# Optimization experiments

Hardware: AMD Instinct MI355X
Metric: run time of the kernel (lower is better)

## Reference

```python
import jax, jax.numpy as jnp
import numpy as np

DIM = 1024
N_HEADS = 16
HEAD_DIM = DIM // N_HEADS  # 64
HALF = HEAD_DIM // 2       # 32
DEPTH = 6
N_BRANCH = 2
NEG_INF = -1e9


def _rot_H(x, cos, sin, m):
    # H direction: adjacent-pair complex layout (..., HALF, 2)
    # x: [B,S,H,D], cos/sin: [HALF], m: [B,S] int
    B, S, H, D = x.shape
    xr = x.reshape(B, S, H, HALF, 2)
    re, im = xr[..., 0], xr[..., 1]
    re2 = re * cos - im * sin
    im2 = re * sin + im * cos
    rot = jnp.stack([re2, im2], axis=-1).reshape(B, S, H, D)
    return jnp.where((m != 0)[:, :, None, None], rot, x)


def _rot_B(x, cos, sin, m):
    # B direction: split-half complex layout (real = first half, imag = second half)
    re, im = x[..., :HALF], x[..., HALF:]
    re2 = re * cos - im * sin
    im2 = re * sin + im * cos
    rot = jnp.concatenate([re2, im2], axis=-1)
    return jnp.where((m != 0)[:, :, None, None], rot, x)


def _apply_rope_instructions(x, H_mask, B_mask, freqs_cos, freqs_sin):
    # Sequentially compose rotations per depth level, as in the torch loops.
    for i in range(DEPTH):
        x = _rot_H(x, freqs_cos[1], freqs_sin[1], H_mask[i])
        for b in range(N_BRANCH):
            x = _rot_B(x, freqs_cos[b + 1], freqs_sin[b + 1], B_mask[i, b])
    return x


def setup_inputs() -> dict:
    key = jax.random.key(0)
    ks = jax.random.split(key, 10)
    B, S = 2, 1024
    x = jax.random.normal(ks[0], (B, S, DIM), dtype=jnp.float32)
    masks = jax.random.randint(ks[1], (B, 1, S, S), 0, 2, dtype=jnp.int32)
    H_mask = jax.random.randint(ks[2], (DEPTH, B, S), 0, 2, dtype=jnp.int32)
    B_mask = jax.random.randint(ks[3], (DEPTH, N_BRANCH, B, S), 0, 2, dtype=jnp.int32)
    theta = jax.random.uniform(ks[4], (4, HALF), dtype=jnp.float32) * 2.0 * np.pi
    freqs_cos = jnp.cos(theta)
    freqs_sin = jnp.sin(theta)
    scale = 1.0 / np.sqrt(DIM)
    wq = jax.random.normal(ks[5], (DIM, DIM), dtype=jnp.float32) * scale
    wk = jax.random.normal(ks[6], (DIM, DIM), dtype=jnp.float32) * scale
    wv = jax.random.normal(ks[7], (DIM, DIM), dtype=jnp.float32) * scale
    wo = jax.random.normal(ks[8], (DIM, DIM), dtype=jnp.float32) * scale
    return {"x": x, "masks": masks, "H_mask": H_mask, "B_mask": B_mask,
            "freqs_cos": freqs_cos, "freqs_sin": freqs_sin,
            "wq": wq, "wk": wk, "wv": wv, "wo": wo}


def reference(x, masks, H_mask, B_mask, freqs_cos, freqs_sin, wq, wk, wv, wo):
    B, S, _ = x.shape
    xq = (x @ wq).reshape(B, S, N_HEADS, HEAD_DIM)
    xk = (x @ wk).reshape(B, S, N_HEADS, HEAD_DIM)
    xv = (x @ wv).reshape(B, S, N_HEADS, HEAD_DIM)
    xq = _apply_rope_instructions(xq, H_mask, B_mask, freqs_cos, freqs_sin)
    xk = _apply_rope_instructions(xk, H_mask, B_mask, freqs_cos, freqs_sin)
    scores = jnp.einsum('bqhd,bkhd->bhqk', xq, xk) / np.sqrt(HEAD_DIM)
    scores = jnp.where(masks == 0, NEG_INF, scores)
    probs = jax.nn.softmax(scores, axis=-1)
    out = jnp.einsum('bhqk,bkhd->bqhd', probs, xv).reshape(B, S, DIM)
    return out @ wo
```

## Files before the change

### kernel.cpp

```cpp
#include <hip/hip_runtime.h>

#define SLEN 1024
#define BATCH 2
#define DEPTH 6

typedef _Float16 h8 __attribute__((ext_vector_type(8)));
typedef float    f4 __attribute__((ext_vector_type(4)));
#define MF16(a, b, c) __builtin_amdgcn_mfma_f32_16x16x32_f16(a, b, c, 0, 0, 0)

#define SW(row, c) ((((c) ^ ((row) & 7))) * 8)

__device__ __forceinline__ void async_cp16(const _Float16* g, _Float16* l) {
  __builtin_amdgcn_global_load_lds(
      (const __attribute__((address_space(1))) void*)g,
      (__attribute__((address_space(3))) void*)l, 16, 0, 0);
}

__global__ __launch_bounds__(256) void prep(const float* __restrict__ x,
    const float* __restrict__ wq, const float* __restrict__ wk,
    const float* __restrict__ wv, const float* __restrict__ wo,
    const int* __restrict__ masks, _Float16* __restrict__ xh,
    _Float16* __restrict__ qt, _Float16* __restrict__ kt,
    _Float16* __restrict__ vt, _Float16* __restrict__ ot,
    unsigned int* __restrict__ mpk) {
  __shared__ _Float16 T[64][72];
  const int bid = blockIdx.x, t = threadIdx.x;
  if (bid < 1024) {
    int idx = (bid * 256 + t) * 8;
    float4 f0 = *(const float4*)(x + idx);
    float4 f1 = *(const float4*)(x + idx + 4);
    union { h8 v; _Float16 e[8]; } u;
    u.e[0] = (_Float16)f0.x; u.e[1] = (_Float16)f0.y;
    u.e[2] = (_Float16)f0.z; u.e[3] = (_Float16)f0.w;
    u.e[4] = (_Float16)f1.x; u.e[5] = (_Float16)f1.y;
    u.e[6] = (_Float16)f1.z; u.e[7] = (_Float16)f1.w;
    *(h8*)(xh + idx) = u.v;
  } else if (bid < 2048) {
    const int i = bid - 1024;
    const int wsel = i >> 8;
    const float* W = wsel == 0 ? wq : wsel == 1 ? wk : wsel == 2 ? wv : wo;
    _Float16* O = wsel == 0 ? qt : wsel == 1 ? kt : wsel == 2 ? vt : ot;
    const int k0 = ((i >> 4) & 15) * 64, n0 = (i & 15) * 64;
    const int rr = t >> 2, cs = (t & 3) * 16;
    #pragma unroll
    for (int j = 0; j < 4; ++j) {
      float4 f = *(const float4*)(W + (size_t)(k0 + rr) * 1024 + n0 + cs + j * 4);
      T[rr][cs + j * 4 + 0] = (_Float16)f.x;
      T[rr][cs + j * 4 + 1] = (_Float16)f.y;
      T[rr][cs + j * 4 + 2] = (_Float16)f.z;
      T[rr][cs + j * 4 + 3] = (_Float16)f.w;
    }
    __syncthreads();
    const int n = t >> 2, ks = (t & 3) * 16;
    union { h8 v; _Float16 e[8]; } u0, u1;
    #pragma unroll
    for (int j = 0; j < 8; ++j) { u0.e[j] = T[ks + j][n]; u1.e[j] = T[ks + 8 + j][n]; }
    *(h8*)(O + (size_t)(n0 + n) * 1024 + k0 + ks)     = u0.v;
    *(h8*)(O + (size_t)(n0 + n) * 1024 + k0 + ks + 8) = u1.v;
  } else {
    const int g = (bid - 2048) * 256 + t;
    const int row = g >> 5, w = g & 31;
    const int* m = masks + (size_t)row * 1024 + w * 32;
    unsigned int bits = 0;
    #pragma unroll
    for (int j4 = 0; j4 < 8; ++j4) {
      int4 mm = *(const int4*)(m + j4 * 4);
      if (mm.x) bits |= 1u << (j4 * 4 + 0);
      if (mm.y) bits |= 1u << (j4 * 4 + 1);
      if (mm.z) bits |= 1u << (j4 * 4 + 2);
      if (mm.w) bits |= 1u << (j4 * 4 + 3);
    }
    mpk[g] = bits;
  }
}

template <int TMODE, typename CT>
__device__ __forceinline__ void gemm16(const _Float16* __restrict__ A,
                                       const _Float16* __restrict__ Bt,
                                       CT* __restrict__ C,
                                       _Float16* __restrict__ SH) {
  _Float16* As = SH;
  _Float16* Bs = SH + 4096;
  const int t    = threadIdx.x;
  const int bm   = blockIdx.y * 64, bn = blockIdx.x * 128;
  const int w    = t >> 6, lane = t & 63;
  const int ln15 = lane & 15, quad = lane >> 4;
  const int wm   = (w >> 1) * 32, wn = (w & 1) * 64;

  const int srow8 = lane >> 3;
  const int sch   = (lane & 7) ^ srow8;
  const _Float16* agp = A  + (size_t)(bm + w * 16 + srow8) * 1024 + sch * 8;
  const _Float16* bgp = Bt + (size_t)(bn + w * 32 + srow8) * 1024 + sch * 8;

  f4 acc[2][4];
  #pragma unroll
  for (int i = 0; i < 2; ++i)
    #pragma unroll
    for (int j = 0; j < 4; ++j) acc[i][j] = (f4){0.f, 0.f, 0.f, 0.f};

  for (int k0 = 0; k0 < 1024; k0 += 64) {
    #pragma unroll
    for (int j = 0; j < 2; ++j)
      async_cp16(agp + k0 + j * 8192, As + w * 1024 + j * 512);
    #pragma unroll
    for (int j = 0; j < 4; ++j)
      async_cp16(bgp + k0 + j * 8192, Bs + w * 2048 + j * 512);
    __syncthreads();
    #pragma unroll
    for (int kk = 0; kk < 8; kk += 4) {
      h8 af[2], bf[4];
      #pragma unroll
      for (int i = 0; i < 2; ++i) {
        int row = wm + i * 16 + ln15;
        af[i] = *(const h8*)&As[row * 64 + SW(row, kk + quad)];
      }
      #pragma unroll
      for (int j = 0; j < 4; ++j) {
        int row = wn + j * 16 + ln15;
        bf[j] = *(const h8*)&Bs[row * 64 + SW(row, kk + quad)];
      }
      #pragma unroll
      for (int i = 0; i < 2; ++i)
        #pragma unroll
        for (int j = 0; j < 4; ++j)
          acc[i][j] = MF16(af[i], bf[j], acc[i][j]);
    }
    __syncthreads();
  }

  if (TMODE == 0) {
    #pragma unroll
    for (int i = 0; i < 2; ++i) {
      int row = bm + wm + i * 16 + quad * 4;
      #pragma unroll
      for (int r = 0; r < 4; ++r)
        #pragma unroll
        for (int j = 0; j < 4; ++j)
          C[(size_t)(row + r) * 1024 + bn + wn + j * 16 + ln15] = (CT)acc[i][j][r];
    }
  } else {
    #pragma unroll
    for (int i = 0; i < 2; ++i) {
      int m0 = bm + wm + i * 16 + quad * 4;
      #pragma unroll
      for (int r = 0; r < 4; ++r) {
        int m = m0 + r;
        size_t base = ((size_t)(m >> 10) * 1024) * 1024 + (m & 1023);
        #pragma unroll
        for (int j = 0; j < 4; ++j)
          C[base + (size_t)(bn + wn + j * 16 + ln15) * 1024] = (CT)acc[i][j][r];
      }
    }
  }
}

__global__ __launch_bounds__(256) void gemm_qkv16(
    const _Float16* __restrict__ xh, const _Float16* __restrict__ qt,
    const _Float16* __restrict__ kt, const _Float16* __restrict__ vtw,
    _Float16* __restrict__ q, _Float16* __restrict__ k,
    _Float16* __restrict__ vth) {
  __shared__ _Float16 SH[12288];
  if (blockIdx.z == 2)      gemm16<1, _Float16>(xh, vtw, vth, SH);
  else if (blockIdx.z == 1) gemm16<0, _Float16>(xh, kt, k, SH);
  else                      gemm16<0, _Float16>(xh, qt, q, SH);
}

__global__ __launch_bounds__(256) void gemm_o16(
    const _Float16* __restrict__ A, const _Float16* __restrict__ Bt,
    float* __restrict__ C) {
  __shared__ _Float16 SH[12288];
  gemm16<0, float>(A, Bt, C, SH);
}

__global__ __launch_bounds__(256) void rope_kernel(_Float16* __restrict__ qf,
    _Float16* __restrict__ kf, const int* __restrict__ Hm,
    const int* __restrict__ Bm, const float* __restrict__ fc,
    const float* __restrict__ fs) {
  __shared__ float c1[32], s1[32], c2[32], s2[32];
  const int t = threadIdx.x;
  if (t < 32) {
    c1[t] = fc[32 + t]; s1[t] = fs[32 + t];
    c2[t] = fc[64 + t]; s2[t] = fs[64 + t];
  }
  __syncthreads();
  const int gid = blockIdx.x * 256 + t;
  const int bs  = gid >> 4;
  _Float16* base = (blockIdx.y == 0 ? qf : kf) + (size_t)gid * 64;
  float vv[64];
  #pragma unroll
  for (int i = 0; i < 8; ++i) {
    union { h8 v; _Float16 e[8]; } u;
    u.v = *(const h8*)(base + i * 8);
    #pragma unroll
    for (int j = 0; j < 8; ++j) vv[i * 8 + j] = (float)u.e[j];
  }
  #pragma unroll 1
  for (int d = 0; d < DEPTH; ++d) {
    if (Hm[d * (BATCH * SLEN) + bs] != 0) {
      #pragma unroll
      for (int j = 0; j < 32; ++j) {
        float re = vv[2 * j], im = vv[2 * j + 1];
        vv[2 * j]     = re * c1[j] - im * s1[j];
        vv[2 * j + 1] = re * s1[j] + im * c1[j];
      }
    }
    if (Bm[(d * 2 + 0) * (BATCH * SLEN) + bs] != 0) {
      #pragma unroll
      for (int j = 0; j < 32; ++j) {
        float re = vv[j], im = vv[j + 32];
        vv[j]      = re * c1[j] - im * s1[j];
        vv[j + 32] = re * s1[j] + im * c1[j];
      }
    }
    if (Bm[(d * 2 + 1) * (BATCH * SLEN) + bs] != 0) {
      #pragma unroll
      for (int j = 0; j < 32; ++j) {
        float re = vv[j], im = vv[j + 32];
        vv[j]      = re * c2[j] - im * s2[j];
        vv[j + 32] = re * s2[j] + im * c2[j];
      }
    }
  }
  #pragma unroll
  for (int i = 0; i < 8; ++i) {
    union { h8 v; _Float16 e[8]; } u;
    #pragma unroll
    for (int j = 0; j < 8; ++j) u.e[j] = (_Float16)vv[i * 8 + j];
    *(h8*)(base + i * 8) = u.v;
  }
}

__global__ __launch_bounds__(256) void attn_mfma(const _Float16* __restrict__ qh,
    const _Float16* __restrict__ kh, const _Float16* __restrict__ vth,
    const unsigned int* __restrict__ mpk, _Float16* __restrict__ out) {
  __shared__ _Float16 Ks[2][64 * 64];
  __shared__ _Float16 Vs[2][64 * 64];
  __shared__ _Float16 QP[4][16][72];

  const int t    = threadIdx.x;
  const int w    = t >> 6, lane = t & 63;
  const int ln15 = lane & 15, quad = lane >> 4;

  const int bh = blockIdx.x & 31;
  const int s0 = (blockIdx.x >> 5) * 64;
  const int b = bh >> 4, h = bh & 15;
  const size_t qkbase = (size_t)b * (SLEN * 1024) + h * 64;
  const size_t vbase  = ((size_t)b * 1024 + h * 64) * SLEN;

  {
    const int srow = t >> 2, sc0 = (t & 3) * 16;
    const _Float16* src = qh + qkbase + (size_t)(s0 + srow) * 1024 + sc0;
    *(h8*)&QP[w][srow & 15][sc0]     = *(const h8*)src;
    *(h8*)&QP[w][srow & 15][sc0 + 8] = *(const h8*)(src + 8);
  }
  h8 aq0 = *(h8*)&QP[w][ln15][quad * 8];
  h8 aq1 = *(h8*)&QP[w][ln15][32 + quad * 8];

  const int srow8 = lane >> 3;
  const int sch   = (lane & 7) ^ srow8;
  const _Float16* kgp = kh + qkbase + (size_t)(w * 16 + srow8) * 1024 + sch * 8;
  const _Float16* vgp = vth + vbase + (size_t)(w * 16 + srow8) * 1024 + sch * 8;

  const unsigned int* mp = mpk + ((size_t)b * SLEN + s0 + w * 16 + quad * 4) * 32;

  float lrow[4] = {1e-30f, 1e-30f, 1e-30f, 1e-30f};
  f4 oacc[4];
  #pragma unroll
  for (int f = 0; f < 4; ++f) oacc[f] = (f4){0.f, 0.f, 0.f, 0.f};

  async_cp16(kgp,        &Ks[0][w * 1024]);
  async_cp16(kgp + 8192, &Ks[0][w * 1024 + 512]);
  async_cp16(vgp,        &Vs[0][w * 1024]);
  async_cp16(vgp + 8192, &Vs[0][w * 1024 + 512]);
  unsigned int w0[4], w1[4];
  #pragma unroll
  for (int r = 0; r < 4; ++r) { w0[r] = mp[r * 32]; w1[r] = mp[r * 32 + 1]; }
  __syncthreads();

  for (int c = 0; c < 16; ++c) {
    const int cur = c & 1;
    unsigned int nw0[4], nw1[4];
    if (c < 15) {
      const size_t ko = (size_t)((c + 1) * 64) * 1024;
      const int    vo = (c + 1) * 64;
      async_cp16(kgp + ko,        &Ks[cur ^ 1][w * 1024]);
      async_cp16(kgp + ko + 8192, &Ks[cur ^ 1][w * 1024 + 512]);
      async_cp16(vgp + vo,        &Vs[cur ^ 1][w * 1024]);
      async_cp16(vgp + vo + 8192, &Vs[cur ^ 1][w * 1024 + 512]);
      #pragma unroll
      for (int r = 0; r < 4; ++r) {
        nw0[r] = mp[r * 32 + (c + 1) * 2];
        nw1[r] = mp[r * 32 + (c + 1) * 2 + 1];
      }
    }

    f4 s[4];
    #pragma unroll
    for (int f = 0; f < 4; ++f) {
      int row = f * 16 + ln15;
      h8 bk0 = *(const h8*)&Ks[cur][row * 64 + SW(row, quad)];
      h8 bk1 = *(const h8*)&Ks[cur][row * 64 + SW(row, 4 + quad)];
      f4 acc = (f4){0.f, 0.f, 0.f, 0.f};
      acc = MF16(aq0, bk0, acc);
      acc = MF16(aq1, bk1, acc);
      s[f] = acc;
    }
    #pragma unroll
    for (int f = 0; f < 4; ++f) {
      const int col = f * 16 + ln15;
      #pragma unroll
      for (int r = 0; r < 4; ++r) {
        unsigned int wd = (col & 32) ? w1[r] : w0[r];
        float p = ((wd >> (col & 31)) & 1u)
                    ? __expf(s[f][r] * 0.125f - 3.0f) : 0.0f;
        lrow[r] += p;
        QP[w][quad * 4 + r][col] = (_Float16)p;
      }
    }
    h8 ap0 = *(h8*)&QP[w][ln15][quad * 8];
    h8 ap1 = *(h8*)&QP[w][ln15][32 + quad * 8];
    #pragma unroll
    for (int f = 0; f < 4; ++f) {
      int row = f * 16 + ln15;
      h8 bv0 = *(const h8*)&Vs[cur][row * 64 + SW(row, quad)];
      h8 bv1 = *(const h8*)&Vs[cur][row * 64 + SW(row, 4 + quad)];
      f4 o = oacc[f];
      o = MF16(ap0, bv0, o);
      o = MF16(ap1, bv1, o);
      oacc[f] = o;
    }
    if (c < 15) {
      #pragma unroll
      for (int r = 0; r < 4; ++r) { w0[r] = nw0[r]; w1[r] = nw1[r]; }
    }
    __syncthreads();
  }

  #pragma unroll
  for (int r = 0; r < 4; ++r) {
    float sm = lrow[r];
    sm += __shfl_xor(sm, 1);
    sm += __shfl_xor(sm, 2);
    sm += __shfl_xor(sm, 4);
    sm += __shfl_xor(sm, 8);
    lrow[r] = 1.0f / sm;
  }
  #pragma unroll
  for (int f = 0; f < 4; ++f)
    #pragma unroll
    for (int r = 0; r < 4; ++r)
      QP[w][quad * 4 + r][f * 16 + ln15] = (_Float16)(oacc[f][r] * lrow[r]);
  const int orow = lane >> 2, oseg = (lane & 3) * 16;
  _Float16* op = out + qkbase + (size_t)(s0 + w * 16 + orow) * 1024 + oseg;
  *(h8*)op       = *(h8*)&QP[w][orow][oseg];
  *(h8*)(op + 8) = *(h8*)&QP[w][orow][oseg + 8];
}

extern "C" void kernel_launch(void* const* d_in, const int* in_sizes, int n_in,
                              void* d_out, int out_size, void* d_ws, size_t ws_size,
                              hipStream_t stream) {
  const float* x     = (const float*)d_in[0];
  const int*   masks = (const int*)d_in[1];
  const int*   Hm    = (const int*)d_in[2];
  const int*   Bm    = (const int*)d_in[3];
  const float* fc    = (const float*)d_in[4];
  const float* fs    = (const float*)d_in[5];
  const float* wq    = (const float*)d_in[6];
  const float* wk    = (const float*)d_in[7];
  const float* wv    = (const float*)d_in[8];
  const float* wo    = (const float*)d_in[9];
  float* out = (float*)d_out;

  _Float16* xh   = (_Float16*)d_ws;
  _Float16* wqt  = xh + (1 << 21);
  _Float16* wkt  = wqt + (1 << 20);
  _Float16* wvt  = wkt + (1 << 20);
  _Float16* wot  = wvt + (1 << 20);
  _Float16* qhh  = wot + (1 << 20);
  _Float16* khh  = qhh + (1 << 21);
  _Float16* vth  = khh + (1 << 21);
  _Float16* aoh  = vth + (1 << 21);
  unsigned int* mpk = (unsigned int*)(aoh + (1 << 21));

  dim3 blk(256);
  prep<<<dim3(2304), blk, 0, stream>>>(x, wq, wk, wv, wo, masks,
                                       xh, wqt, wkt, wvt, wot, mpk);
  gemm_qkv16<<<dim3(8, 32, 3), blk, 0, stream>>>(xh, wqt, wkt, wvt,
                                                 qhh, khh, vth);
  rope_kernel<<<dim3(128, 2), blk, 0, stream>>>(qhh, khh, Hm, Bm, fc, fs);
  attn_mfma<<<dim3(512), blk, 0, stream>>>(qhh, khh, vth, mpk, aoh);
  gemm_o16<<<dim3(8, 32), blk, 0, stream>>>(aoh, wot, out);
}
```

Measured before the change: 166.5 us.

## Fuse RoPE rotations into QKV GEMM epilogue via LDS staging

Removes the separate rope kernel and applies the depth-composed H/B rotations inside the Q and K GEMM epilogue. Accumulators are staged into swizzled shared memory, then each thread owns half of one head's row (4 threads per row covering two heads) and applies the rotations in registers before a vectorized store. This saves a kernel launch and a full read and write of Q and K in global memory. In exchange the GEMM epilogue gets longer, with extra LDS traffic and a sync, and register pressure rises.

```diff
diff --git a/kernel.cpp b/kernel.cpp
--- a/kernel.cpp
+++ b/kernel.cpp
@@ -78,7 +78,10 @@
 __device__ __forceinline__ void gemm16(const _Float16* __restrict__ A,
                                        const _Float16* __restrict__ Bt,
                                        CT* __restrict__ C,
-                                       _Float16* __restrict__ SH) {
+                                       const int* __restrict__ Hm,
+                                       const int* __restrict__ Bm,
+                                       _Float16* __restrict__ SH,
+                                       const float* __restrict__ FR) {
   _Float16* As = SH;
   _Float16* Bs = SH + 4096;
   const int t    = threadIdx.x;
@@ -138,7 +141,7 @@
         for (int j = 0; j < 4; ++j)
           C[(size_t)(row + r) * 1024 + bn + wn + j * 16 + ln15] = (CT)acc[i][j][r];
     }
-  } else {
+  } else if (TMODE == 1) {
     #pragma unroll
     for (int i = 0; i < 2; ++i) {
       int m0 = bm + wm + i * 16 + quad * 4;
@@ -150,6 +153,75 @@
         for (int j = 0; j < 4; ++j)
           C[base + (size_t)(bn + wn + j * 16 + ln15) * 1024] = (CT)acc[i][j][r];
       }
+    }
+  } else {
+    _Float16* EP = SH;
+    #pragma unroll
+    for (int i = 0; i < 2; ++i)
+      #pragma unroll
+      for (int j = 0; j < 4; ++j) {
+        int cl = wn + j * 16 + ln15;
+        #pragma unroll
+        for (int r = 0; r < 4; ++r) {
+          int rl = wm + i * 16 + quad * 4 + r;
+          EP[rl * 128 + (((cl >> 3) ^ (rl & 15)) << 3) + (cl & 7)] =
+              (_Float16)acc[i][j][r];
+        }
+      }
+    __syncthreads();
+    const int row = t >> 2, head = (t >> 1) & 1, p = t & 1;
+    const int bs = bm + row;
+    const int r15 = row & 15;
+    float vv[32];
+    #pragma unroll
+    for (int cc = 0; cc < 4; ++cc) {
+      int lc = head * 8 + 2 * p + (cc & 1) + (cc >> 1) * 4;
+      union { h8 v; _Float16 e[8]; } u;
+      u.v = *(const h8*)&EP[row * 128 + (lc ^ r15) * 8];
+      #pragma unroll
+      for (int e = 0; e < 8; ++e) vv[cc * 8 + e] = (float)u.e[e];
+    }
+    #pragma unroll 1
+    for (int d = 0; d < DEPTH; ++d) {
+      if (Hm[d * (BATCH * SLEN) + bs] != 0) {
+        #pragma unroll
+        for (int jj = 0; jj < 8; ++jj) {
+          int j0 = 8 * p + jj, j1 = 16 + 8 * p + jj;
+          float re0 = vv[2 * jj], im0 = vv[2 * jj + 1];
+          vv[2 * jj]     = re0 * FR[j0] - im0 * FR[32 + j0];
+          vv[2 * jj + 1] = re0 * FR[32 + j0] + im0 * FR[j0];
+          float re1 = vv[16 + 2 * jj], im1 = vv[17 + 2 * jj];
+          vv[16 + 2 * jj] = re1 * FR[j1] - im1 * FR[32 + j1];
+          vv[17 + 2 * jj] = re1 * FR[32 + j1] + im1 * FR[j1];
+        }
+      }
+      if (Bm[(d * 2 + 0) * (BATCH * SLEN) + bs] != 0) {
+        #pragma unroll
+        for (int jj = 0; jj < 16; ++jj) {
+          int j = 16 * p + jj;
+          float re = vv[jj], im = vv[16 + jj];
+          vv[jj]      = re * FR[j] - im * FR[32 + j];
+          vv[16 + jj] = re * FR[32 + j] + im * FR[j];
+        }
+      }
+      if (Bm[(d * 2 + 1) * (BATCH * SLEN) + bs] != 0) {
+        #pragma unroll
+        for (int jj = 0; jj < 16; ++jj) {
+          int j = 16 * p + jj;
+          float re = vv[jj], im = vv[16 + jj];
+          vv[jj]      = re * FR[64 + j] - im * FR[96 + j];
+          vv[16 + jj] = re * FR[96 + j] + im * FR[64 + j];
+        }
+      }
+    }
+    _Float16* dst = (_Float16*)C + (size_t)(bm + row) * 1024 + bn + head * 64;
+    #pragma unroll
+    for (int cc = 0; cc < 4; ++cc) {
+      union { h8 v; _Float16 e[8]; } u;
+      #pragma unroll
+      for (int e = 0; e < 8; ++e) u.e[e] = (_Float16)vv[cc * 8 + e];
+      int off = (cc < 2) ? (16 * p + cc * 8) : (32 + 16 * p + (cc - 2) * 8);
+      *(h8*)(dst + off) = u.v;
     }
   }
 }
@@ -158,76 +230,30 @@
     const _Float16* __restrict__ xh, const _Float16* __restrict__ qt,
     const _Float16* __restrict__ kt, const _Float16* __restrict__ vtw,
     _Float16* __restrict__ q, _Float16* __restrict__ k,
-    _Float16* __restrict__ vth) {
+    _Float16* __restrict__ vth, const int* __restrict__ Hm,
+    const int* __restrict__ Bm, const float* __restrict__ fc,
+    const float* __restrict__ fs) {
   __shared__ _Float16 SH[12288];
-  if (blockIdx.z == 2)      gemm16<1, _Float16>(xh, vtw, vth, SH);
-  else if (blockIdx.z == 1) gemm16<0, _Float16>(xh, kt, k, SH);
-  else                      gemm16<0, _Float16>(xh, qt, q, SH);
+  __shared__ float FR[128];
+  if (blockIdx.z != 2 && threadIdx.x < 128) {
+    int g = threadIdx.x & 31;
+    FR[threadIdx.x] = (threadIdx.x < 32) ? fc[32 + g]
+                    : (threadIdx.x < 64) ? fs[32 + g]
+                    : (threadIdx.x < 96) ? fc[64 + g] : fs[64 + g];
+  }
+  if (blockIdx.z == 2)
+    gemm16<1, _Float16>(xh, vtw, vth, nullptr, nullptr, SH, nullptr);
+  else if (blockIdx.z == 1)
+    gemm16<2, _Float16>(xh, kt, k, Hm, Bm, SH, FR);
+  else
+    gemm16<2, _Float16>(xh, qt, q, Hm, Bm, SH, FR);
 }
 
 __global__ __launch_bounds__(256) void gemm_o16(
     const _Float16* __restrict__ A, const _Float16* __restrict__ Bt,
     float* __restrict__ C) {
   __shared__ _Float16 SH[12288];
-  gemm16<0, float>(A, Bt, C, SH);
-}
-
-__global__ __launch_bounds__(256) void rope_kernel(_Float16* __restrict__ qf,
-    _Float16* __restrict__ kf, const int* __restrict__ Hm,
-    const int* __restrict__ Bm, const float* __restrict__ fc,
-    const float* __restrict__ fs) {
-  __shared__ float c1[32], s1[32], c2[32], s2[32];
-  const int t = threadIdx.x;
-  if (t < 32) {
-    c1[t] = fc[32 + t]; s1[t] = fs[32 + t];
-    c2[t] = fc[64 + t]; s2[t] = fs[64 + t];
-  }
-  __syncthreads();
-  const int gid = blockIdx.x * 256 + t;
-  const int bs  = gid >> 4;
-  _Float16* base = (blockIdx.y == 0 ? qf : kf) + (size_t)gid * 64;
-  float vv[64];
-  #pragma unroll
-  for (int i = 0; i < 8; ++i) {
-    union { h8 v; _Float16 e[8]; } u;
-    u.v = *(const h8*)(base + i * 8);
-    #pragma unroll
-    for (int j = 0; j < 8; ++j) vv[i * 8 + j] = (float)u.e[j];
-  }
-  #pragma unroll 1
-  for (int d = 0; d < DEPTH; ++d) {
-    if (Hm[d * (BATCH * SLEN) + bs] != 0) {
-      #pragma unroll
-      for (int j = 0; j < 32; ++j) {
-        float re = vv[2 * j], im = vv[2 * j + 1];
-        vv[2 * j]     = re * c1[j] - im * s1[j];
-        vv[2 * j + 1] = re * s1[j] + im * c1[j];
-      }
-    }
-    if (Bm[(d * 2 + 0) * (BATCH * SLEN) + bs] != 0) {
-      #pragma unroll
-      for (int j = 0; j < 32; ++j) {
-        float re = vv[j], im = vv[j + 32];
-        vv[j]      = re * c1[j] - im * s1[j];
-        vv[j + 32] = re * s1[j] + im * c1[j];
-      }
-    }
-    if (Bm[(d * 2 + 1) * (BATCH * SLEN) + bs] != 0) {
-      #pragma unroll
-      for (int j = 0; j < 32; ++j) {
-        float re = vv[j], im = vv[j + 32];
-        vv[j]      = re * c2[j] - im * s2[j];
-        vv[j + 32] = re * s2[j] + im * c2[j];
-      }
-    }
-  }
-  #pragma unroll
-  for (int i = 0; i < 8; ++i) {
-    union { h8 v; _Float16 e[8]; } u;
-    #pragma unroll
-    for (int j = 0; j < 8; ++j) u.e[j] = (_Float16)vv[i * 8 + j];
-    *(h8*)(base + i * 8) = u.v;
-  }
+  gemm16<0, float>(A, Bt, C, nullptr, nullptr, SH, nullptr);
 }
 
 __global__ __launch_bounds__(256) void attn_mfma(const _Float16* __restrict__ qh,
@@ -386,8 +412,7 @@
   prep<<<dim3(2304), blk, 0, stream>>>(x, wq, wk, wv, wo, masks,
                                        xh, wqt, wkt, wvt, wot, mpk);
   gemm_qkv16<<<dim3(8, 32, 3), blk, 0, stream>>>(xh, wqt, wkt, wvt,
-                                                 qhh, khh, vth);
-  rope_kernel<<<dim3(128, 2), blk, 0, stream>>>(qhh, khh, Hm, Bm, fc, fs);
+                                                 qhh, khh, vth, Hm, Bm, fc, fs);
   attn_mfma<<<dim3(512), blk, 0, stream>>>(qhh, khh, vth, mpk, aoh);
   gemm_o16<<<dim3(8, 32), blk, 0, stream>>>(aoh, wot, out);
 }
```

After: 158.9 us, median of 2. -4.6%, faster.
